# Kernel optimization log

Measured on AMD Instinct MI355X. Metric: run time of the kernel, lower is better.

Reference implementation:

```python
import jax, jax.numpy as jnp
import numpy as np

B, C, H, W0, W1 = 2, 96, 64, 128, 128
NL, K, R = 2, 4, 6  # num_layers, cross-scan directions, dt_rank = ceil(C/16)
PNAMES = ['norm_w','norm_b','in_proj_w','conv_w','x_proj_w','dt_w','dt_b','A_logs','Ds',
          'out_norm_w','out_norm_b','out_proj_w','norm2_w','norm2_b','fc1_w','fc1_b','fc2_w','fc2_b']


def setup_inputs() -> dict:
    key = jax.random.key(0)
    ks = iter(jax.random.split(key, 40))
    def rn(shape, s=0.02):
        return jax.random.normal(next(ks), shape, jnp.float32) * s
    return dict(
        x0=jax.random.normal(next(ks), (B, C, H, W0), jnp.float32),
        x1=jax.random.normal(next(ks), (B, C, H, W1), jnp.float32),
        norm_w=jnp.ones((NL, C)), norm_b=jnp.zeros((NL, C)),
        in_proj_w=rn((NL, C, C)),                 # SS2D in_proj (Linear2d, bias=False)
        conv_w=rn((NL, C, 1, 3, 3), 0.1),         # depthwise 3x3, bias=False
        x_proj_w=rn((NL, K, R + 2, C)),           # dt_rank + 2*d_state rows (d_state=1)
        dt_w=rn((NL, K, C, R), 0.1),
        dt_b=rn((NL, K, C), 0.1),
        A_logs=jnp.zeros((NL, K, C)),             # v0 init with d_state=1 -> log(1)=0
        Ds=jnp.ones((NL, K, C)),
        out_norm_w=jnp.ones((NL, C)), out_norm_b=jnp.zeros((NL, C)),
        out_proj_w=rn((NL, C, C)),                # bias=False
        norm2_w=jnp.ones((NL, C)), norm2_b=jnp.zeros((NL, C)),
        fc1_w=rn((NL, 4 * C, C)), fc1_b=jnp.zeros((NL, 4 * C)),
        fc2_w=rn((NL, C, 4 * C)), fc2_b=jnp.zeros((NL, C)),
    )


def ln2d(x, w, b, eps=1e-5):
    # LayerNorm2d: normalize over channel dim of NCHW
    mu = x.mean(1, keepdims=True)
    var = ((x - mu) ** 2).mean(1, keepdims=True)
    return (x - mu) * jax.lax.rsqrt(var + eps) * w[None, :, None, None] + b[None, :, None, None]


def conv1x1(x, w):  # Linear2d: w (out,in)
    return jnp.einsum('bchw,dc->bdhw', x, w)


def dwconv3(x, w):  # depthwise 3x3, SAME padding
    return jax.lax.conv_general_dilated(x, w, (1, 1), 'SAME',
        dimension_numbers=('NCHW', 'OIHW', 'NCHW'), feature_group_count=x.shape[1])


def linear_scan(a, b):
    # h_t = a_t * h_{t-1} + b_t along last axis, via associative scan
    def comb(l, r):
        al, bl = l
        ar, br = r
        return (ar * al, ar * bl + br)
    return jax.lax.associative_scan(comb, (a, b), axis=-1)[1]


def ss2d(x, p):
    # SS2Dv2 forward_type='v05_noz', channel_first, d_state=1
    Bs_, Cd, Hh, Ww = x.shape
    Ll = Hh * Ww
    x = conv1x1(x, p['in_proj_w'])
    x = jax.nn.silu(dwconv3(x, p['conv_w']))
    # CrossScan: row-major, col-major, and their flips -> (B,K,C,L)
    xs0 = x.reshape(Bs_, Cd, Ll)
    xs1 = x.transpose(0, 1, 3, 2).reshape(Bs_, Cd, Ll)
    xs = jnp.stack([xs0, xs1, xs0[..., ::-1], xs1[..., ::-1]], 1)
    xdbl = jnp.einsum('bkcl,kdc->bkdl', xs, p['x_proj_w'])
    dts, Bmat, Cmat = xdbl[:, :, :R], xdbl[:, :, R:R + 1], xdbl[:, :, R + 1:R + 2]
    delta = jax.nn.softplus(jnp.einsum('bkrl,kcr->bkcl', dts, p['dt_w']) + p['dt_b'][None, :, :, None])
    A = -jnp.exp(p['A_logs'])                       # (K,C), scalar state
    a = jnp.exp(delta * A[None, :, :, None])        # (B,K,C,L)
    bterm = delta * Bmat * xs                       # Bmat broadcasts over C (d_state=1)
    h = linear_scan(a, bterm)
    ys = Cmat * h + p['Ds'][None, :, :, None] * xs  # (B,K,C,L)
    # CrossMerge: un-flip dirs 2,3; map col-major back to row-major; sum
    y_row = ys[:, 0] + ys[:, 2, :, ::-1]
    y_col = ys[:, 1] + ys[:, 3, :, ::-1]
    y_col = y_col.reshape(Bs_, Cd, Ww, Hh).transpose(0, 1, 3, 2).reshape(Bs_, Cd, Ll)
    y = (y_row + y_col).reshape(Bs_, Cd, Hh, Ww)
    y = ln2d(y, p['out_norm_w'], p['out_norm_b'])
    return conv1x1(y, p['out_proj_w'])


def block(x, p):
    # drop_path is identity in eval mode; all dropout rates are 0
    x = x + ss2d(ln2d(x, p['norm_w'], p['norm_b']), p)
    h = conv1x1(ln2d(x, p['norm2_w'], p['norm2_b']), p['fc1_w']) + p['fc1_b'][None, :, None, None]
    h = jax.nn.gelu(h, approximate=False)
    return x + conv1x1(h, p['fc2_w']) + p['fc2_b'][None, :, None, None]


def run_stack(x, params):
    for i in range(NL):
        p = {k: v[i] for k, v in params.items()}
        x = block(x, p)
    return x


def _forward(x0, x1, params):
    x = jnp.concatenate([x0, x1], -1)
    xb = x[..., ::-1]
    x = run_stack(x, params)
    xb = run_stack(xb, params)
    xbf = xb[..., ::-1]
    w0 = x0.shape[-1]
    y0 = 0.5 * (x[..., :w0] + xbf[..., :w0])
    y1 = 0.5 * (x[..., w0:] + xbf[..., w0:])
    return (y0, y1)


def reference(x0, x1, norm_w, norm_b, in_proj_w, conv_w, x_proj_w, dt_w, dt_b, A_logs, Ds,
              out_norm_w, out_norm_b, out_proj_w, norm2_w, norm2_b, fc1_w, fc1_b, fc2_w, fc2_b):
    params = dict(zip(PNAMES, [norm_w, norm_b, in_proj_w, conv_w, x_proj_w, dt_w, dt_b, A_logs, Ds,
                               out_norm_w, out_norm_b, out_proj_w, norm2_w, norm2_b, fc1_w, fc1_b, fc2_w, fc2_b]))
    return _forward(x0, x1, params)
```

## Files before the change

kernel.cpp:

```cpp
#include <hip/hip_runtime.h>
#include <cstdint>
#include <cstddef>

#define BT 4
#define CC 96
#define HH 64
#define WW 256
#define LL (HH*WW)
#define KD 4
#define RR 6
#define NLAY 2
#define C4 (4*CC)
#define SLOTF 47424
#define STPW 2048

typedef unsigned short u16;
typedef __attribute__((ext_vector_type(8))) short bf16x8;
typedef __attribute__((ext_vector_type(4))) float f32x4;

__device__ __forceinline__ u16 f2bf(float f){
  unsigned u = __float_as_uint(f);
  unsigned r = (u + 0x7FFFu + ((u >> 16) & 1u)) >> 16;
  return (u16)r;
}
__device__ __forceinline__ float bf2f(u16 h){
  return __uint_as_float(((unsigned)h) << 16);
}
__device__ __forceinline__ unsigned pk_bf16(float lo, float hi){
  unsigned r;
  asm volatile("v_cvt_pk_bf16_f32 %0, %1, %2" : "=v"(r) : "v"(lo), "v"(hi));
  return r;
}
__device__ __forceinline__ float fexp2(float x){
  float r; asm("v_exp_f32 %0, %1" : "=v"(r) : "v"(x)); return r;
}
__device__ __forceinline__ float flog2(float x){
  float r; asm("v_log_f32 %0, %1" : "=v"(r) : "v"(x)); return r;
}
__device__ __forceinline__ float gelu_f(float v){
  float t = v*v;
  float u = v*fmaf(0.0356774081f, t, 0.7978845608f);
  float e2 = __expf(2.f*u);
  float r = __builtin_amdgcn_rcpf(e2 + 1.f);
  return fmaf(-v, r, v);
}

__global__ void k_build(const float* __restrict__ x0, const float* __restrict__ x1,
                        float* __restrict__ X){
  size_t i = (size_t)blockIdx.x*256 + threadIdx.x;
  size_t tot = (size_t)2*CC*HH*WW;
  if (i >= tot) return;
  int w = i % WW; size_t r = i / WW;
  int h = r % HH; size_t bc = r / HH;
  float val;
  if (w < 128) val = x0[(bc*HH + h)*128 + w];
  else         val = x1[(bc*HH + h)*128 + (w-128)];
  X[i] = val;
  size_t ib = ((bc + (size_t)2*CC)*HH + h)*WW + (WW-1-w);
  X[ib] = val;
}

template<bool ST, typename T>
__global__ __launch_bounds__(256) void k_pack(const T* __restrict__ src,
      u16* __restrict__ dst, float* __restrict__ st){
  __shared__ float tl[CC][33];
  int tid = threadIdx.x;
  int l0 = blockIdx.x*32, b = blockIdx.y;
  for (int e = tid; e < CC*32; e += 256){
    int c = e >> 5, dl = e & 31;
    T raw = src[((size_t)b*CC + c)*LL + l0 + dl];
    float vv;
    if constexpr (sizeof(T) == 2) vv = bf2f((u16)raw); else vv = (float)raw;
    tl[c][dl] = vv;
  }
  __syncthreads();
  if (ST && tid < 32){
    float s = 0.f, ss = 0.f;
    for (int c = 0; c < CC; ++c){ float vv = tl[c][tid]; s += vv; ss += vv*vv; }
    float mu = s*(1.f/CC);
    float var = ss*(1.f/CC) - mu*mu;
    st[(size_t)b*LL + l0 + tid] = mu;
    st[(size_t)BT*LL + (size_t)b*LL + l0 + tid] = rsqrtf(var + 1e-5f);
  }
  int dl = tid >> 3, cg = tid & 7;
  u16* dp = dst + ((size_t)b*LL + l0 + dl)*104 + cg*12;
  #pragma unroll
  for (int q = 0; q < 3; ++q){
    ushort4 pk;
    pk.x = f2bf(tl[cg*12 + q*4 + 0][dl]);
    pk.y = f2bf(tl[cg*12 + q*4 + 1][dl]);
    pk.z = f2bf(tl[cg*12 + q*4 + 2][dl]);
    pk.w = f2bf(tl[cg*12 + q*4 + 3][dl]);
    *(ushort4*)(dp + q*4) = pk;
  }
}

template<int M, int K, bool FC1ORD, bool LNF, bool BIAS>
__global__ void k_prepw(const float* __restrict__ W, const float* __restrict__ lnw,
      const float* __restrict__ lnb, const float* __restrict__ bias,
      u16* __restrict__ Wb, float* __restrict__ s1, float* __restrict__ cadd){
  int lay = blockIdx.y;
  W += (size_t)lay*M*K;
  Wb += (size_t)lay*SLOTF*2;
  s1 += (size_t)lay*SLOTF;
  cadd += (size_t)lay*SLOTF;
  int m = blockIdx.x*64 + threadIdx.x;
  if (m >= M) return;
  int rowfrag = m >> 4, lr = m & 15;
  float s1v = 0.f, sbv = 0.f;
  for (int c = 0; c < K; ++c){
    float wv = W[(size_t)m*K + c];
    float wf = LNF ? wv*lnw[lay*K + c] : wv;
    u16 h = f2bf(wf);
    int colfrag = c >> 5, lg = (c >> 3) & 3, j = c & 7;
    int f;
    if (FC1ORD) f = (rowfrag/6)*18 + colfrag*6 + (rowfrag % 6);
    else        f = colfrag*(M/16) + rowfrag;
    Wb[(size_t)(f*64 + lg*16 + lr)*8 + j] = h;
    s1v += bf2f(h);
    if (LNF) sbv = fmaf(wv, lnb[lay*K + c], sbv);
  }
  if (BIAS) sbv += bias[lay*M + m];
  s1[m] = s1v;
  cadd[m] = sbv;
}

template<bool LNF, bool RES, bool WF32, bool WBF, bool STATS, bool WPB>
__global__ __launch_bounds__(256) void k_gmm2(
    const u16* __restrict__ Wb, const u16* __restrict__ inT,
    float* __restrict__ outF, u16* __restrict__ outT,
    const float* __restrict__ s1v, const float* __restrict__ cadd,
    const float* __restrict__ res,
    const float* __restrict__ stI, float* __restrict__ stO,
    u16* __restrict__ outPB){
  __shared__ u16 bt[128*104];
  int tid = threadIdx.x, lane = tid & 63, wid = tid >> 6;
  int l0 = blockIdx.x*128;
  int lr = lane & 15, lg = lane >> 4;
  const int4* bsrc = (const int4*)(inT + (size_t)l0*104);
  for (int i = tid; i < 1664; i += 256) ((int4*)bt)[i] = bsrc[i];
  __syncthreads();
  f32x4 acc[6][2];
  #pragma unroll
  for (int mf = 0; mf < 6; ++mf){ acc[mf][0] = (f32x4){0,0,0,0}; acc[mf][1] = (f32x4){0,0,0,0}; }
  #pragma unroll
  for (int ks = 0; ks < 3; ++ks){
    bf16x8 af[6];
    #pragma unroll
    for (int mf = 0; mf < 6; ++mf)
      af[mf] = *(const bf16x8*)(Wb + (size_t)((ks*6 + mf)*64 + lane)*8);
    bf16x8 bfr[2];
    #pragma unroll
    for (int ls = 0; ls < 2; ++ls)
      bfr[ls] = *(const bf16x8*)&bt[(wid*32 + ls*16 + lr)*104 + ks*32 + lg*8];
    #pragma unroll
    for (int mf = 0; mf < 6; ++mf)
      #pragma unroll
      for (int ls = 0; ls < 2; ++ls)
        acc[mf][ls] = __builtin_amdgcn_mfma_f32_16x16x32_bf16(af[mf], bfr[ls], acc[mf][ls], 0, 0, 0);
  }
  #pragma unroll
  for (int ls = 0; ls < 2; ++ls){
    int l = l0 + wid*32 + ls*16 + lr;
    int b = l >> 14, lb = l & (LL-1);
    float mu = 0.f, rs = 0.f;
    if (LNF){ mu = stI[l]; rs = stI[(size_t)BT*LL + l]; }
    float ssum = 0.f, ssq = 0.f;
    #pragma unroll
    for (int mf = 0; mf < 6; ++mf){
      float o[4];
      #pragma unroll
      for (int r = 0; r < 4; ++r){
        int mm = mf*16 + lg*4 + r;
        float vv = acc[mf][ls][r];
        if (LNF) vv = fmaf(rs, vv, fmaf(-mu*rs, s1v[mm], cadd[mm]));
        else     vv += cadd[mm];
        if (RES) vv += res[((size_t)b*96 + mm)*LL + lb];
        if (WF32) outF[((size_t)b*96 + mm)*LL + lb] = vv;
        if (WPB)  outPB[((size_t)b*96 + mm)*LL + lb] = f2bf(vv);
        if (STATS){ ssum += vv; ssq += vv*vv; }
        o[r] = vv;
      }
      if (WBF){
        ushort4 pk;
        pk.x = f2bf(o[0]); pk.y = f2bf(o[1]); pk.z = f2bf(o[2]); pk.w = f2bf(o[3]);
        *(ushort4*)(outT + (size_t)l*104 + mf*16 + lg*4) = pk;
      }
    }
    if (STATS){
      ssum += __shfl_xor(ssum, 16); ssq += __shfl_xor(ssq, 16);
      ssum += __shfl_xor(ssum, 32); ssq += __shfl_xor(ssq, 32);
      if (lane < 16){
        float mu2 = ssum*(1.f/CC);
        float var = ssq*(1.f/CC) - mu2*mu2;
        stO[l] = mu2;
        stO[(size_t)BT*LL + l] = rsqrtf(var + 1e-5f);
      }
    }
  }
}

__global__ __launch_bounds__(512, 4) void k_mlp(
    const u16* __restrict__ Wb1, const u16* __restrict__ Wb2,
    const u16* __restrict__ XT, float* __restrict__ X, u16* __restrict__ XTout,
    const float* __restrict__ s11, const float* __restrict__ c1,
    const float* __restrict__ c2,
    const float* __restrict__ stI, float* __restrict__ stO){
  __shared__ u16 bt[128*104];
  __shared__ u16 hs[128*104];
  int tid = threadIdx.x, lane = tid & 63, wid = tid >> 6;
  int l0 = blockIdx.x*128;
  int lr = lane & 15, lg = lane >> 4;
  const int4* bsrc = (const int4*)(XT + (size_t)l0*104);
  for (int i = tid; i < 1664; i += 512) ((int4*)bt)[i] = bsrc[i];

  int l = l0 + wid*16 + lr;
  float mu = stI[l];
  float rs = stI[(size_t)BT*LL + l];
  float nmr = -mu*rs;
  __syncthreads();

  int hrow = (wid*16 + lr)*104;
  f32x4 acc2[6];
  #pragma unroll
  for (int mf = 0; mf < 6; ++mf) acc2[mf] = (f32x4){0,0,0,0};

  for (int cc = 0; cc < 4; ++cc){
    f32x4 acc1[6];
    #pragma unroll
    for (int mf = 0; mf < 6; ++mf) acc1[mf] = (f32x4){0,0,0,0};
    #pragma unroll
    for (int ks = 0; ks < 3; ++ks){
      bf16x8 af[6];
      #pragma unroll
      for (int mf = 0; mf < 6; ++mf)
        af[mf] = *(const bf16x8*)(Wb1 + (size_t)((cc*18 + ks*6 + mf)*64 + lane)*8);
      bf16x8 bfr = *(const bf16x8*)&bt[hrow + ks*32 + lg*8];
      #pragma unroll
      for (int mf = 0; mf < 6; ++mf)
        acc1[mf] = __builtin_amdgcn_mfma_f32_16x16x32_bf16(af[mf], bfr, acc1[mf], 0, 0, 0);
    }
    #pragma unroll
    for (int mf = 0; mf < 6; ++mf){
      float4 sv = *(const float4*)&s11[cc*96 + mf*16 + lg*4];
      float4 cv = *(const float4*)&c1 [cc*96 + mf*16 + lg*4];
      float g0 = gelu_f(fmaf(rs, acc1[mf][0], fmaf(nmr, sv.x, cv.x)));
      float g1 = gelu_f(fmaf(rs, acc1[mf][1], fmaf(nmr, sv.y, cv.y)));
      float g2 = gelu_f(fmaf(rs, acc1[mf][2], fmaf(nmr, sv.z, cv.z)));
      float g3 = gelu_f(fmaf(rs, acc1[mf][3], fmaf(nmr, sv.w, cv.w)));
      uint2 pw;
      pw.x = pk_bf16(g0, g1);
      pw.y = pk_bf16(g2, g3);
      *(uint2*)&hs[hrow + mf*16 + lg*4] = pw;
    }
    #pragma unroll
    for (int ks = 0; ks < 3; ++ks){
      bf16x8 a2[6];
      #pragma unroll
      for (int mf2 = 0; mf2 < 6; ++mf2)
        a2[mf2] = *(const bf16x8*)(Wb2 + (size_t)(((cc*3 + ks)*6 + mf2)*64 + lane)*8);
      bf16x8 bfr2 = *(const bf16x8*)&hs[hrow + ks*32 + lg*8];
      #pragma unroll
      for (int mf2 = 0; mf2 < 6; ++mf2)
        acc2[mf2] = __builtin_amdgcn_mfma_f32_16x16x32_bf16(a2[mf2], bfr2, acc2[mf2], 0, 0, 0);
    }
  }
  {
    int b = l >> 14, lb = l & (LL-1);
    float ssum = 0.f, ssq = 0.f;
    #pragma unroll
    for (int mf = 0; mf < 6; ++mf){
      float o[4];
      #pragma unroll
      for (int r = 0; r < 4; ++r){
        int mm = mf*16 + lg*4 + r;
        float vv = acc2[mf][r] + c2[mm];
        vv += X[((size_t)b*96 + mm)*LL + lb];
        X[((size_t)b*96 + mm)*LL + lb] = vv;
        ssum += vv; ssq += vv*vv;
        o[r] = vv;
      }
      ushort4 pk;
      pk.x = f2bf(o[0]); pk.y = f2bf(o[1]); pk.z = f2bf(o[2]); pk.w = f2bf(o[3]);
      *(ushort4*)(XTout + (size_t)l*104 + mf*16 + lg*4) = pk;
    }
    ssum += __shfl_xor(ssum, 16); ssq += __shfl_xor(ssq, 16);
    ssum += __shfl_xor(ssum, 32); ssq += __shfl_xor(ssq, 32);
    if (lane < 16){
      float mu2 = ssum*(1.f/CC);
      float var = ssq*(1.f/CC) - mu2*mu2;
      stO[l] = mu2;
      stO[(size_t)BT*LL + l] = rsqrtf(var + 1e-5f);
    }
  }
}

__global__ __launch_bounds__(256) void k_dwconv_silu_t(const u16* __restrict__ u,
      u16* __restrict__ v, u16* __restrict__ vT, const float* __restrict__ cw){
  __shared__ float tl[32][33];
  int bc = blockIdx.z;
  int c = bc % CC;
  int w0 = blockIdx.x*32, h0 = blockIdx.y*32;
  const u16* up = u + (size_t)bc*LL;
  const float* k9 = cw + c*9;
  int t = threadIdx.x;
  int wl = (t & 7)*4, hl = t >> 3;
  int h = h0 + hl, w = w0 + wl;
  float acc[4] = {0.f,0.f,0.f,0.f};
  #pragma unroll
  for (int dh = -1; dh <= 1; ++dh){
    int h2 = h + dh;
    if (h2 < 0 || h2 >= HH) continue;
    const u16* row = up + (size_t)h2*WW + w;
    ushort4 mq = *(const ushort4*)row;
    float m0 = bf2f(mq.x), m1 = bf2f(mq.y), m2 = bf2f(mq.z), m3 = bf2f(mq.w);
    float lft = (w > 0) ? bf2f(row[-1]) : 0.f;
    float rgt = (w + 4 < WW) ? bf2f(row[4]) : 0.f;
    float k0 = k9[(dh+1)*3], k1 = k9[(dh+1)*3+1], k2 = k9[(dh+1)*3+2];
    acc[0] += lft*k0 + m0*k1 + m1*k2;
    acc[1] += m0*k0 + m1*k1 + m2*k2;
    acc[2] += m1*k0 + m2*k1 + m3*k2;
    acc[3] += m2*k0 + m3*k1 + rgt*k2;
  }
  float s[4];
  #pragma unroll
  for (int j = 0; j < 4; ++j){
    float a = acc[j];
    float e = __expf(-a);
    s[j] = a * __builtin_amdgcn_rcpf(1.f + e);
    tl[wl + j][hl] = s[j];
  }
  uint2 pw;
  pw.x = pk_bf16(s[0], s[1]);
  pw.y = pk_bf16(s[2], s[3]);
  *(uint2*)&v[(size_t)bc*LL + (size_t)h*WW + w] = pw;
  __syncthreads();
  int ww = t >> 3, hh4 = (t & 7)*4;
  uint2 po;
  po.x = pk_bf16(tl[ww][hh4],   tl[ww][hh4+1]);
  po.y = pk_bf16(tl[ww][hh4+2], tl[ww][hh4+3]);
  *(uint2*)&vT[(size_t)bc*LL + (size_t)(w0 + ww)*HH + h0 + hh4] = po;
}

__global__ void k_xproj(const u16* __restrict__ v, const u16* __restrict__ vT,
                        float* __restrict__ G, const float* __restrict__ xpw){
  int which = blockIdx.y;
  const u16* src = which ? vT : v;
  int kA = which ? 1 : 0, kB = which ? 3 : 2;
  size_t i = (size_t)blockIdx.x*256 + threadIdx.x;
  if (i >= (size_t)BT*LL) return;
  int b = (int)(i / LL), l = (int)(i % LL);
  const u16* sp = src + (size_t)b*CC*LL + l;
  const float* wA = xpw + (size_t)kA*8*CC;
  const float* wB = xpw + (size_t)kB*8*CC;
  float aA[8], aB[8];
  #pragma unroll
  for (int d = 0; d < 8; ++d){ aA[d] = 0.f; aB[d] = 0.f; }
  for (int c = 0; c < CC; ++c){
    float xv = bf2f(sp[(size_t)c*LL]);
    #pragma unroll
    for (int d = 0; d < 8; ++d){
      aA[d] = fmaf(wA[d*CC + c], xv, aA[d]);
      aB[d] = fmaf(wB[d*CC + c], xv, aB[d]);
    }
  }
  float* gA = G + (((size_t)b*KD + kA)*8)*LL + l;
  float* gB = G + (((size_t)b*KD + kB)*8)*LL + l;
  #pragma unroll
  for (int d = 0; d < 8; ++d){ gA[(size_t)d*LL] = aA[d]; gB[(size_t)d*LL] = aB[d]; }
}

__device__ __forceinline__ void ld4(const float* p, float* o){
  float4 t = *(const float4*)p; o[0]=t.x; o[1]=t.y; o[2]=t.z; o[3]=t.w;
}
__device__ __forceinline__ void ldb4(const u16* p, float* o){
  ushort4 t = *(const ushort4*)p;
  o[0]=bf2f(t.x); o[1]=bf2f(t.y); o[2]=bf2f(t.z); o[3]=bf2f(t.w);
}
__device__ __forceinline__ void rev4(float* a){
  float t0 = a[0]; a[0] = a[3]; a[3] = t0;
  float t1 = a[1]; a[1] = a[2]; a[2] = t1;
}

__global__ __launch_bounds__(256) void k_scan3(const float* __restrict__ G,
                       const u16* __restrict__ v, const u16* __restrict__ vT,
                       u16* __restrict__ Y,
                       const float* __restrict__ dtw_, const float* __restrict__ dtb_,
                       const float* __restrict__ Alog_, const float* __restrict__ Ds_){
  const size_t SZ = (size_t)BT*CC*LL;
  const float LOG2E = 1.4426950408889634f, LN2 = 0.6931471805599453f;
  int wid = threadIdx.x >> 6, lane = threadIdx.x & 63;
  int tile = blockIdx.x*4 + wid;
  int sy = blockIdx.y;
  bool rev = (blockIdx.z != 0);
  int c = sy % CC; int t2 = sy / CC; int kk = t2 & 1; int b = t2 >> 1;
  int k = (rev ? 2 : 0) + kk;
  const u16* src = (kk ? vT : v) + ((size_t)b*CC + c)*LL;
  const float* g = G + (((size_t)b*KD + k)*8)*LL;
  float dtw[RR];
  #pragma unroll
  for (int r = 0; r < RR; ++r) dtw[r] = dtw_[((size_t)k*CC + c)*RR + r];
  float dtb = dtb_[k*CC + c];
  float A  = -__expf(Alog_[k*CC + c]);
  float Dv = Ds_[k*CC + c];
  u16* yout = Y + (size_t)k*SZ + ((size_t)b*CC + c)*LL;

  int lstore0 = tile*STPW;
  float carry = 0.f;
  for (int p = 0; p < 1 + STPW/256; ++p){
    int base = lstore0 - 256 + p*256;
    if (base < 0) continue;
    bool st = (base >= lstore0);
    int l = base + (lane<<2);
    int ga = rev ? (LL-4-l) : l;
    float r0[4], r1[4], r2[4], r3[4], r4[4], r5[4], g6b[4], g7b[4], xb[4];
    ld4(g + 0*(size_t)LL + ga, r0);
    ld4(g + 1*(size_t)LL + ga, r1);
    ld4(g + 2*(size_t)LL + ga, r2);
    ld4(g + 3*(size_t)LL + ga, r3);
    ld4(g + 4*(size_t)LL + ga, r4);
    ld4(g + 5*(size_t)LL + ga, r5);
    ld4(g + 6*(size_t)LL + ga, g6b);
    if (st) ld4(g + 7*(size_t)LL + ga, g7b);
    else { g7b[0]=0.f; g7b[1]=0.f; g7b[2]=0.f; g7b[3]=0.f; }
    ldb4(src + ga, xb);
    if (rev){
      rev4(r0); rev4(r1); rev4(r2); rev4(r3); rev4(r4); rev4(r5);
      rev4(g6b); rev4(g7b); rev4(xb);
    }
    float av[4], bt[4];
    #pragma unroll
    for (int i = 0; i < 4; ++i){
      float dsum = dtb;
      dsum = fmaf(r0[i], dtw[0], dsum);
      dsum = fmaf(r1[i], dtw[1], dsum);
      dsum = fmaf(r2[i], dtw[2], dsum);
      dsum = fmaf(r3[i], dtw[3], dsum);
      dsum = fmaf(r4[i], dtw[4], dsum);
      dsum = fmaf(r5[i], dtw[5], dsum);
      float dl2 = dsum*LOG2E;
      float y = flog2(1.f + fexp2(dl2));
      y = (dsum > 20.f) ? dl2 : y;
      float delta = y*LN2;
      av[i] = fexp2(A*y);
      bt[i] = delta * g6b[i] * xb[i];
    }
    float P = av[0], Q = bt[0];
    #pragma unroll
    for (int i = 1; i < 4; ++i){ Q = fmaf(av[i], Q, bt[i]); P *= av[i]; }
    #pragma unroll
    for (int off = 1; off < 64; off <<= 1){
      float Pp = __shfl_up(P, (unsigned)off);
      float Qp = __shfl_up(Q, (unsigned)off);
      if (lane >= off){ Q = fmaf(P, Qp, Q); P *= Pp; }
    }
    float Pe = __shfl_up(P, 1u), Qe = __shfl_up(Q, 1u);
    if (lane == 0){ Pe = 1.f; Qe = 0.f; }
    float h = fmaf(Pe, carry, Qe);
    if (st){
      float ys[4];
      #pragma unroll
      for (int i = 0; i < 4; ++i){
        h = fmaf(av[i], h, bt[i]);
        ys[i] = fmaf(g7b[i], h, Dv*xb[i]);
      }
      carry = __shfl(h, 63);
      if (rev) rev4(ys);
      uint2 pw;
      pw.x = pk_bf16(ys[0], ys[1]);
      pw.y = pk_bf16(ys[2], ys[3]);
      *(uint2*)&yout[ga] = pw;
    } else {
      #pragma unroll
      for (int i = 0; i < 4; ++i) h = fmaf(av[i], h, bt[i]);
      carry = __shfl(h, 63);
    }
  }
}

__global__ __launch_bounds__(256) void k_combine4(const u16* __restrict__ Y, u16* __restrict__ z){
  const size_t SZ = (size_t)BT*CC*LL;
  __shared__ float tl[64][65];
  int bc = blockIdx.z;
  int w0 = blockIdx.x*64;
  int t = threadIdx.x;
  const u16* y1p = Y + SZ   + (size_t)bc*LL;
  const u16* y3p = Y + 3*SZ + (size_t)bc*LL;
  {
    int wl = t >> 2;
    int h0 = (t & 3)*16;
    size_t base = (size_t)(w0 + wl)*HH + h0;
    #pragma unroll
    for (int j = 0; j < 4; ++j){
      ushort4 a = *(const ushort4*)&y1p[base + j*4];
      ushort4 bq = *(const ushort4*)&y3p[base + j*4];
      tl[wl][h0 + j*4 + 0] = bf2f(a.x) + bf2f(bq.x);
      tl[wl][h0 + j*4 + 1] = bf2f(a.y) + bf2f(bq.y);
      tl[wl][h0 + j*4 + 2] = bf2f(a.z) + bf2f(bq.z);
      tl[wl][h0 + j*4 + 3] = bf2f(a.w) + bf2f(bq.w);
    }
  }
  __syncthreads();
  const u16* y0p = Y +        (size_t)bc*LL;
  const u16* y2p = Y + 2*SZ + (size_t)bc*LL;
  u16* zp = z + (size_t)bc*LL;
  {
    int h = t >> 2;
    int wq = (t & 3)*16;
    #pragma unroll
    for (int j = 0; j < 4; ++j){
      int wl = wq + j*4;
      size_t idx = (size_t)h*WW + w0 + wl;
      ushort4 a = *(const ushort4*)&y0p[idx];
      ushort4 bq = *(const ushort4*)&y2p[idx];
      ushort4 o;
      o.x = f2bf(bf2f(a.x) + bf2f(bq.x) + tl[wl+0][h]);
      o.y = f2bf(bf2f(a.y) + bf2f(bq.y) + tl[wl+1][h]);
      o.z = f2bf(bf2f(a.z) + bf2f(bq.z) + tl[wl+2][h]);
      o.w = f2bf(bf2f(a.w) + bf2f(bq.w) + tl[wl+3][h]);
      *(ushort4*)&zp[idx] = o;
    }
  }
}

__global__ void k_output(const float* __restrict__ X, float* __restrict__ out){
  size_t i = (size_t)blockIdx.x*256 + threadIdx.x;
  size_t half = (size_t)2*CC*HH*128;
  if (i >= half) return;
  int w = i % 128; size_t r = i / 128;
  int h = r % HH; size_t bc = r / HH;
  size_t fwd = (bc*HH + h)*WW;
  size_t bwd = ((bc + (size_t)2*CC)*HH + h)*WW;
  out[i]        = 0.5f*(X[fwd + w]       + X[bwd + (WW-1-w)]);
  out[half + i] = 0.5f*(X[fwd + 128 + w] + X[bwd + (127 - w)]);
}

extern "C" void kernel_launch(void* const* d_in, const int* in_sizes, int n_in,
                              void* d_out, int out_size, void* d_ws, size_t ws_size,
                              hipStream_t stream){
  const float* x0        = (const float*)d_in[0];
  const float* x1        = (const float*)d_in[1];
  const float* norm_w    = (const float*)d_in[2];
  const float* norm_b    = (const float*)d_in[3];
  const float* in_proj_w = (const float*)d_in[4];
  const float* conv_w    = (const float*)d_in[5];
  const float* x_proj_w  = (const float*)d_in[6];
  const float* dt_w      = (const float*)d_in[7];
  const float* dt_b      = (const float*)d_in[8];
  const float* A_logs    = (const float*)d_in[9];
  const float* Ds        = (const float*)d_in[10];
  const float* out_norm_w= (const float*)d_in[11];
  const float* out_norm_b= (const float*)d_in[12];
  const float* out_proj_w= (const float*)d_in[13];
  const float* norm2_w   = (const float*)d_in[14];
  const float* norm2_b   = (const float*)d_in[15];
  const float* fc1_w     = (const float*)d_in[16];
  const float* fc1_b     = (const float*)d_in[17];
  const float* fc2_w     = (const float*)d_in[18];
  const float* fc2_b     = (const float*)d_in[19];

  const size_t SZ = (size_t)BT*CC*LL;
  float* X  = (float*)d_ws;
  float* t  = X + SZ;
  float* u  = t + SZ;
  float* G  = u + SZ;
  float* v  = G + (size_t)BT*KD*8*LL;
  float* vT = v + SZ;
  float* Yf = vT + SZ;
  u16*   Yb = (u16*)Yf;
  u16*   XT = (u16*)Yf;
  u16*   uB = (u16*)u;
  u16*   vB = (u16*)v;
  u16*   vTB= (u16*)vT;
  u16*   tB = (u16*)t;
  u16*   tT = (u16*)u;
  float* ext = Yf + 4*SZ;
  float* stats_X = ext;
  float* stats_t = stats_X + 2*(size_t)BT*LL;
  float* wsl     = stats_t + 2*(size_t)BT*LL;

  float* p0 = wsl;
  u16*  WbI0 = (u16*)p0;          float* s1I0 = p0 + 4608;  float* cI0 = p0 + 4704;
  u16*  WbO0 = (u16*)(p0+4800);   float* s1O0 = p0 + 9408;  float* cO0 = p0 + 9504;
  u16*  Wb10 = (u16*)(p0+9600);   float* s110 = p0 + 28032; float* c10 = p0 + 28416;
  u16*  Wb20 = (u16*)(p0+28800);  float* s120 = p0 + 47232; float* c20 = p0 + 47328;

  k_prepw<96,96,false,true,false><<<dim3(2,NLAY),64,0,stream>>>(in_proj_w, norm_w, norm_b, nullptr, WbI0, s1I0, cI0);
  k_prepw<96,96,false,true,false><<<dim3(2,NLAY),64,0,stream>>>(out_proj_w, out_norm_w, out_norm_b, nullptr, WbO0, s1O0, cO0);
  k_prepw<384,96,true,true,true><<<dim3(6,NLAY),64,0,stream>>>(fc1_w, norm2_w, norm2_b, fc1_b, Wb10, s110, c10);
  k_prepw<96,384,false,false,true><<<dim3(2,NLAY),64,0,stream>>>(fc2_w, nullptr, nullptr, fc2_b, Wb20, s120, c20);

  k_build<<<(2*CC*HH*WW + 255)/256, 256, 0, stream>>>(x0, x1, X);
  k_pack<true,float><<<dim3(LL/32, BT), 256, 0, stream>>>(X, XT, stats_X);

  for (int lay = 0; lay < NLAY; ++lay){
    size_t so = (size_t)lay*SLOTF;
    const u16* WbI = WbI0 + so*2; const float* s1I = s1I0 + so; const float* cI = cI0 + so;
    const u16* WbO = WbO0 + so*2; const float* s1O = s1O0 + so; const float* cO = cO0 + so;
    const u16* Wb1 = Wb10 + so*2; const float* s11 = s110 + so; const float* c1 = c10 + so;
    const u16* Wb2 = Wb20 + so*2; const float* c2 = c20 + so;
    const float* cw  = conv_w    + (size_t)lay*CC*9;
    const float* xpw = x_proj_w  + (size_t)lay*KD*8*CC;
    const float* dw  = dt_w      + (size_t)lay*KD*CC*RR;
    const float* db  = dt_b      + (size_t)lay*KD*CC;
    const float* Al  = A_logs    + (size_t)lay*KD*CC;
    const float* Dp  = Ds        + (size_t)lay*KD*CC;

    k_gmm2<true,false,false,false,false,true><<<dim3(BT*LL/128),256,0,stream>>>(
        WbI, XT, nullptr, nullptr, s1I, cI, nullptr, stats_X, nullptr, uB);
    k_dwconv_silu_t<<<dim3(8,2,BT*CC), 256, 0, stream>>>(uB, vB, vTB, cw);
    k_xproj<<<dim3(BT*LL/256, 2), 256, 0, stream>>>(vB, vTB, G, xpw);
    k_scan3<<<dim3(2,768,2), 256, 0, stream>>>(G, vB, vTB, Yb, dw, db, Al, Dp);
    k_combine4<<<dim3(4,1,BT*CC), 256, 0, stream>>>(Yb, tB);
    k_pack<true,u16><<<dim3(LL/32, BT), 256, 0, stream>>>(tB, tT, stats_t);
    k_gmm2<true,true,true,true,true,false><<<dim3(BT*LL/128),256,0,stream>>>(
        WbO, tT, X, XT, s1O, cO, X, stats_t, stats_X, nullptr);
    k_mlp<<<dim3(BT*LL/128),512,0,stream>>>(
        Wb1, Wb2, XT, X, XT, s11, c1, c2, stats_X, stats_X);
  }

  k_output<<<(unsigned)(((size_t)2*CC*HH*128 + 255)/256), 256, 0, stream>>>(X, (float*)d_out);
}
```

Measured before the change: 421.0 us.

## Store x_proj output in bf16 and widen scan to 8 elements per lane

The x_proj projections G are now written as bf16 instead of fp32, which halves the traffic between k_xproj and k_scan3. The scan processes 8 elements per lane, so each wave covers chunks of 512. Each wave now owns a 4096-long segment, so only one block is launched per sequence along x, and each segment still warms up from the previous 512-element chunk. Fewer, longer segments cut redundant warm-up work, at the cost of fewer waves and lower bf16 precision for dt, B and C.

```diff
diff --git a/kernel.cpp b/kernel.cpp
--- a/kernel.cpp
+++ b/kernel.cpp
@@ -12,7 +12,8 @@
 #define NLAY 2
 #define C4 (4*CC)
 #define SLOTF 47424
-#define STPW 2048
+#define STPW 4096
+#define WARM 512
 
 typedef unsigned short u16;
 typedef __attribute__((ext_vector_type(8))) short bf16x8;
@@ -343,7 +344,7 @@
 }
 
 __global__ void k_xproj(const u16* __restrict__ v, const u16* __restrict__ vT,
-                        float* __restrict__ G, const float* __restrict__ xpw){
+                        u16* __restrict__ G, const float* __restrict__ xpw){
   int which = blockIdx.y;
   const u16* src = which ? vT : v;
   int kA = which ? 1 : 0, kB = which ? 3 : 2;
@@ -364,25 +365,25 @@
       aB[d] = fmaf(wB[d*CC + c], xv, aB[d]);
     }
   }
-  float* gA = G + (((size_t)b*KD + kA)*8)*LL + l;
-  float* gB = G + (((size_t)b*KD + kB)*8)*LL + l;
-  #pragma unroll
-  for (int d = 0; d < 8; ++d){ gA[(size_t)d*LL] = aA[d]; gB[(size_t)d*LL] = aB[d]; }
-}
-
-__device__ __forceinline__ void ld4(const float* p, float* o){
-  float4 t = *(const float4*)p; o[0]=t.x; o[1]=t.y; o[2]=t.z; o[3]=t.w;
-}
-__device__ __forceinline__ void ldb4(const u16* p, float* o){
-  ushort4 t = *(const ushort4*)p;
-  o[0]=bf2f(t.x); o[1]=bf2f(t.y); o[2]=bf2f(t.z); o[3]=bf2f(t.w);
-}
-__device__ __forceinline__ void rev4(float* a){
-  float t0 = a[0]; a[0] = a[3]; a[3] = t0;
-  float t1 = a[1]; a[1] = a[2]; a[2] = t1;
-}
-
-__global__ __launch_bounds__(256) void k_scan3(const float* __restrict__ G,
+  u16* gA = G + (((size_t)b*KD + kA)*8)*LL + l;
+  u16* gB = G + (((size_t)b*KD + kB)*8)*LL + l;
+  #pragma unroll
+  for (int d = 0; d < 8; ++d){ gA[(size_t)d*LL] = f2bf(aA[d]); gB[(size_t)d*LL] = f2bf(aB[d]); }
+}
+
+__device__ __forceinline__ void ldbf8(const u16* p, float* o){
+  uint4 t = *(const uint4*)p;
+  o[0]=bf2f((u16)(t.x & 0xffff)); o[1]=bf2f((u16)(t.x >> 16));
+  o[2]=bf2f((u16)(t.y & 0xffff)); o[3]=bf2f((u16)(t.y >> 16));
+  o[4]=bf2f((u16)(t.z & 0xffff)); o[5]=bf2f((u16)(t.z >> 16));
+  o[6]=bf2f((u16)(t.w & 0xffff)); o[7]=bf2f((u16)(t.w >> 16));
+}
+__device__ __forceinline__ void rev8(float* a){
+  #pragma unroll
+  for (int i = 0; i < 4; ++i){ float t0 = a[i]; a[i] = a[7-i]; a[7-i] = t0; }
+}
+
+__global__ __launch_bounds__(256) void k_scan3(const u16* __restrict__ G,
                        const u16* __restrict__ v, const u16* __restrict__ vT,
                        u16* __restrict__ Y,
                        const float* __restrict__ dtw_, const float* __restrict__ dtb_,
@@ -390,13 +391,13 @@
   const size_t SZ = (size_t)BT*CC*LL;
   const float LOG2E = 1.4426950408889634f, LN2 = 0.6931471805599453f;
   int wid = threadIdx.x >> 6, lane = threadIdx.x & 63;
-  int tile = blockIdx.x*4 + wid;
+  int tile = wid;
   int sy = blockIdx.y;
   bool rev = (blockIdx.z != 0);
   int c = sy % CC; int t2 = sy / CC; int kk = t2 & 1; int b = t2 >> 1;
   int k = (rev ? 2 : 0) + kk;
   const u16* src = (kk ? vT : v) + ((size_t)b*CC + c)*LL;
-  const float* g = G + (((size_t)b*KD + k)*8)*LL;
+  const u16* g = G + (((size_t)b*KD + k)*8)*LL;
   float dtw[RR];
   #pragma unroll
   for (int r = 0; r < RR; ++r) dtw[r] = dtw_[((size_t)k*CC + c)*RR + r];
@@ -407,47 +408,44 @@
 
   int lstore0 = tile*STPW;
   float carry = 0.f;
-  for (int p = 0; p < 1 + STPW/256; ++p){
-    int base = lstore0 - 256 + p*256;
+  for (int p = 0; p < 1 + STPW/WARM; ++p){
+    int base = lstore0 - WARM + p*WARM;
     if (base < 0) continue;
     bool st = (base >= lstore0);
-    int l = base + (lane<<2);
-    int ga = rev ? (LL-4-l) : l;
-    float r0[4], r1[4], r2[4], r3[4], r4[4], r5[4], g6b[4], g7b[4], xb[4];
-    ld4(g + 0*(size_t)LL + ga, r0);
-    ld4(g + 1*(size_t)LL + ga, r1);
-    ld4(g + 2*(size_t)LL + ga, r2);
-    ld4(g + 3*(size_t)LL + ga, r3);
-    ld4(g + 4*(size_t)LL + ga, r4);
-    ld4(g + 5*(size_t)LL + ga, r5);
-    ld4(g + 6*(size_t)LL + ga, g6b);
-    if (st) ld4(g + 7*(size_t)LL + ga, g7b);
-    else { g7b[0]=0.f; g7b[1]=0.f; g7b[2]=0.f; g7b[3]=0.f; }
-    ldb4(src + ga, xb);
-    if (rev){
-      rev4(r0); rev4(r1); rev4(r2); rev4(r3); rev4(r4); rev4(r5);
-      rev4(g6b); rev4(g7b); rev4(xb);
-    }
-    float av[4], bt[4];
-    #pragma unroll
-    for (int i = 0; i < 4; ++i){
-      float dsum = dtb;
-      dsum = fmaf(r0[i], dtw[0], dsum);
-      dsum = fmaf(r1[i], dtw[1], dsum);
-      dsum = fmaf(r2[i], dtw[2], dsum);
-      dsum = fmaf(r3[i], dtw[3], dsum);
-      dsum = fmaf(r4[i], dtw[4], dsum);
-      dsum = fmaf(r5[i], dtw[5], dsum);
-      float dl2 = dsum*LOG2E;
+    int l = base + (lane<<3);
+    int ga = rev ? (LL-8-l) : l;
+    float dsum[8], g6b[8], g7b[8], xb[8];
+    #pragma unroll
+    for (int i = 0; i < 8; ++i) dsum[i] = dtb;
+    #pragma unroll
+    for (int r = 0; r < RR; ++r){
+      float t8[8];
+      ldbf8(g + (size_t)r*LL + ga, t8);
+      #pragma unroll
+      for (int i = 0; i < 8; ++i) dsum[i] = fmaf(t8[i], dtw[r], dsum[i]);
+    }
+    ldbf8(g + (size_t)6*LL + ga, g6b);
+    if (st){
+      ldbf8(g + (size_t)7*LL + ga, g7b);
+    } else {
+      #pragma unroll
+      for (int i = 0; i < 8; ++i) g7b[i] = 0.f;
+    }
+    ldbf8(src + ga, xb);
+    if (rev){ rev8(dsum); rev8(g6b); rev8(g7b); rev8(xb); }
+    float av[8], bt[8];
+    #pragma unroll
+    for (int i = 0; i < 8; ++i){
+      float dl2 = dsum[i]*LOG2E;
       float y = flog2(1.f + fexp2(dl2));
-      y = (dsum > 20.f) ? dl2 : y;
+      y = (dsum[i] > 20.f) ? dl2 : y;
       float delta = y*LN2;
       av[i] = fexp2(A*y);
       bt[i] = delta * g6b[i] * xb[i];
     }
     float P = av[0], Q = bt[0];
     #pragma unroll
-    for (int i = 1; i < 4; ++i){ Q = fmaf(av[i], Q, bt[i]); P *= av[i]; }
+    for (int i = 1; i < 8; ++i){ Q = fmaf(av[i], Q, bt[i]); P *= av[i]; }
     #pragma unroll
     for (int off = 1; off < 64; off <<= 1){
       float Pp = __shfl_up(P, (unsigned)off);
@@ -458,21 +456,23 @@
     if (lane == 0){ Pe = 1.f; Qe = 0.f; }
     float h = fmaf(Pe, carry, Qe);
     if (st){
-      float ys[4];
-      #pragma unroll
-      for (int i = 0; i < 4; ++i){
+      float ys[8];
+      #pragma unroll
+      for (int i = 0; i < 8; ++i){
         h = fmaf(av[i], h, bt[i]);
         ys[i] = fmaf(g7b[i], h, Dv*xb[i]);
       }
       carry = __shfl(h, 63);
-      if (rev) rev4(ys);
-      uint2 pw;
+      if (rev) rev8(ys);
+      uint4 pw;
       pw.x = pk_bf16(ys[0], ys[1]);
       pw.y = pk_bf16(ys[2], ys[3]);
-      *(uint2*)&yout[ga] = pw;
+      pw.z = pk_bf16(ys[4], ys[5]);
+      pw.w = pk_bf16(ys[6], ys[7]);
+      *(uint4*)&yout[ga] = pw;
     } else {
       #pragma unroll
-      for (int i = 0; i < 4; ++i) h = fmaf(av[i], h, bt[i]);
+      for (int i = 0; i < 8; ++i) h = fmaf(av[i], h, bt[i]);
       carry = __shfl(h, 63);
     }
   }
@@ -567,6 +567,7 @@
   float* v  = G + (size_t)BT*KD*8*LL;
   float* vT = v + SZ;
   float* Yf = vT + SZ;
+  u16*   Gb = (u16*)G;
   u16*   Yb = (u16*)Yf;
   u16*   XT = (u16*)Yf;
   u16*   uB = (u16*)u;
@@ -609,8 +610,8 @@
     k_gmm2<true,false,false,false,false,true><<<dim3(BT*LL/128),256,0,stream>>>(
         WbI, XT, nullptr, nullptr, s1I, cI, nullptr, stats_X, nullptr, uB);
     k_dwconv_silu_t<<<dim3(8,2,BT*CC), 256, 0, stream>>>(uB, vB, vTB, cw);
-    k_xproj<<<dim3(BT*LL/256, 2), 256, 0, stream>>>(vB, vTB, G, xpw);
-    k_scan3<<<dim3(2,768,2), 256, 0, stream>>>(G, vB, vTB, Yb, dw, db, Al, Dp);
+    k_xproj<<<dim3(BT*LL/256, 2), 256, 0, stream>>>(vB, vTB, Gb, xpw);
+    k_scan3<<<dim3(1,768,2), 256, 0, stream>>>(Gb, vB, vTB, Yb, dw, db, Al, Dp);
     k_combine4<<<dim3(4,1,BT*CC), 256, 0, stream>>>(Yb, tB);
     k_pack<true,u16><<<dim3(LL/32, BT), 256, 0, stream>>>(tB, tT, stats_t);
     k_gmm2<true,true,true,true,true,false><<<dim3(BT*LL/128),256,0,stream>>>(
```

Result: faster. 403.4 us (-4.2%).
